# Kernel optimization log

Hardware: AMD Instinct MI355X
Metric: run time of the kernel (lower is better)

## Reference

```python
import jax, jax.numpy as jnp
import numpy as np

NEG = -1e30  # stands in for -inf on the diagonal; exp(NEG - max) == 0 exactly


def setup_inputs() -> dict:
    key = jax.random.key(0)
    k1, k2, k3, k4, k5 = jax.random.split(key, 5)
    B, C, H, W = 4, 512, 128, 128
    mid = C // 8  # 64
    x = jax.random.normal(k1, (B, C, H, W), dtype=jnp.float32)
    Wq = jax.random.normal(k2, (mid, C), dtype=jnp.float32) * (1.0 / np.sqrt(C))
    Wk = jax.random.normal(k3, (mid, C), dtype=jnp.float32) * (1.0 / np.sqrt(C))
    Wv = jax.random.normal(k4, (C, C), dtype=jnp.float32) * (1.0 / np.sqrt(C))
    gamma = jax.random.normal(k5, (1,), dtype=jnp.float32) * 0.1
    return {"x": x, "Wq": Wq, "Wk": Wk, "Wv": Wv, "gamma": gamma}


def reference(x, Wq, Wk, Wv, gamma):
    B, C, H, W = x.shape
    # 1x1 convs == channel matmuls
    q = jnp.einsum('bchw,mc->bmhw', x, Wq)  # (B, mid, H, W)
    k = jnp.einsum('bchw,mc->bmhw', x, Wk)
    v = jnp.einsum('bchw,dc->bdhw', x, Wv)  # (B, C, H, W)

    # vertical (H-axis) logits with -inf diagonal: eH[b,i,w,j] = sum_m q[b,m,i,w] k[b,m,j,w]
    eH = jnp.einsum('bmiw,bmjw->biwj', q, k)           # (B, H, W, H)
    diag = jnp.eye(H, dtype=bool)[:, None, :]          # (H, 1, H)
    eH = jnp.where(diag, NEG, eH)

    # horizontal (W-axis) logits: eW[b,h,i,j] = sum_m q[b,m,h,i] k[b,m,h,j]
    eW = jnp.einsum('bmhi,bmhj->bhij', q, k)           # (B, H, W, W)

    # joint softmax over the concatenated H+W logits
    attn = jax.nn.softmax(jnp.concatenate([eH, eW], axis=3), axis=3)  # (B, H, W, H+W)
    aH = attn[:, :, :, :H]  # (B, H, W, H)
    aW = attn[:, :, :, H:]  # (B, H, W, W)

    # attention-weighted value aggregation along each axis
    outH = jnp.einsum('bcjw,biwj->bciw', v, aH)  # (B, C, H, W)
    outW = jnp.einsum('bchj,bhij->bchi', v, aW)  # (B, C, H, W)

    return gamma[0] * (outH + outW) + x
```

## Files before the change

kernel.cpp:

```cpp
#include <hip/hip_runtime.h>
#include <cstdint>
#include <cstddef>

#define NEGV (-1e30f)

constexpr int C_ = 512, H_ = 128, W_ = 128;
constexpr int P_ = 16384;

typedef short bf16x8 __attribute__((ext_vector_type(8)));
typedef float f32x4  __attribute__((ext_vector_type(4)));
typedef _Float16 f16x4 __attribute__((ext_vector_type(4)));
#define MFMA16(a, b, c) __builtin_amdgcn_mfma_f32_16x16x32_bf16((a), (b), (c), 0, 0, 0)

#define SWZ128(r, cs) (((r) << 7) + (((((cs) >> 3) ^ ((r) & 7))) << 3) + ((cs) & 7))
#define SWZ64(r, cs)  (((r) << 6) + (((((cs) >> 3) ^ ((r) & 7))) << 3) + ((cs) & 7))

__device__ inline void gl_lds16(const void* g, void* l) {
    __builtin_amdgcn_global_load_lds(
        (const __attribute__((address_space(1))) unsigned int*)g,
        (__attribute__((address_space(3))) unsigned int*)l, 16, 0, 0);
}

__device__ inline unsigned short f2bf(float f) {
    union { float f; uint32_t i; } t; t.f = f;
    uint32_t r = t.i + 0x7FFFu + ((t.i >> 16) & 1u);
    return (unsigned short)(r >> 16);
}

__global__ __launch_bounds__(256) void kwconv(
    const float* __restrict__ Wq, const float* __restrict__ Wk,
    const float* __restrict__ Wv,
    unsigned short* __restrict__ Wqkbf, unsigned short* __restrict__ Wvbf)
{
    const int i4 = (blockIdx.x * 256 + threadIdx.x) * 4;
    const float* src; unsigned short* dst; int off;
    if (i4 < 32768)       { src = Wq + i4;          dst = Wqkbf + i4; }
    else if (i4 < 65536)  { off = i4 - 32768; src = Wk + off; dst = Wqkbf + i4; }
    else                  { off = i4 - 65536; src = Wv + off; dst = Wvbf + off; }
    const float4 v = *(const float4*)src;
    ushort4 u; u.x = f2bf(v.x); u.y = f2bf(v.y); u.z = f2bf(v.z); u.w = f2bf(v.w);
    *(ushort4*)dst = u;
}

__global__ __launch_bounds__(256) void kprep1(
    const float* __restrict__ x, unsigned short* __restrict__ xTbf)
{
    __shared__ float t[32][33];
    const int tid = threadIdx.x;
    const int h0 = (blockIdx.x >> 2) * 32, w0 = (blockIdx.x & 3) * 32;
    const size_t base = (size_t)blockIdx.y * P_;
    {
        const int r = tid >> 3, c4 = (tid & 7) * 4;
        const float4 v = *(const float4*)&x[base + (size_t)(h0 + r) * 128 + w0 + c4];
        t[r][c4] = v.x; t[r][c4 + 1] = v.y; t[r][c4 + 2] = v.z; t[r][c4 + 3] = v.w;
    }
    __syncthreads();
    {
        const int wr = tid >> 3, hc = (tid & 7) * 4;
        ushort4 u;
        u.x = f2bf(t[hc][wr]);     u.y = f2bf(t[hc + 1][wr]);
        u.z = f2bf(t[hc + 2][wr]); u.w = f2bf(t[hc + 3][wr]);
        *(ushort4*)&xTbf[base + (size_t)(w0 + wr) * 128 + h0 + hc] = u;
    }
}

__global__ __launch_bounds__(256) void kprep2(
    const float* __restrict__ x, unsigned short* __restrict__ xbfT)
{
    __shared__ float t[32][33];
    const int tid = threadIdx.x;
    const int p0 = blockIdx.x * 32, c0 = blockIdx.y * 32, b = blockIdx.z;
    {
        const int r = tid >> 3, c4 = (tid & 7) * 4;
        const float4 v = *(const float4*)&x[((size_t)(b * C_ + c0 + r)) * P_ + p0 + c4];
        t[r][c4] = v.x; t[r][c4 + 1] = v.y; t[r][c4 + 2] = v.z; t[r][c4 + 3] = v.w;
    }
    __syncthreads();
    {
        const int pr = tid >> 3, cc = (tid & 7) * 4;
        ushort4 u;
        u.x = f2bf(t[cc][pr]);     u.y = f2bf(t[cc + 1][pr]);
        u.z = f2bf(t[cc + 2][pr]); u.w = f2bf(t[cc + 3][pr]);
        *(ushort4*)&xbfT[((size_t)b * P_ + p0 + pr) * C_ + c0 + cc] = u;
    }
}

__global__ __launch_bounds__(256) void kgemmqk(
    const unsigned short* __restrict__ A, const unsigned short* __restrict__ Bm,
    unsigned short* __restrict__ outbf)
{
    __shared__ __attribute__((aligned(16))) unsigned short sA[2][128 * 64];
    __shared__ __attribute__((aligned(16))) unsigned short sB[2][128 * 64];
    const int tid = threadIdx.x;
    const int pbase = blockIdx.x * 128, b = blockIdx.z;
    const int lane = tid & 63, wv = tid >> 6;
    const int m0 = (wv >> 1) * 64, p0 = (wv & 1) * 64;
    const int fr = lane & 15, fq = lane >> 4;

    f32x4 acc[4][4];
#pragma unroll
    for (int i = 0; i < 4; i++)
#pragma unroll
        for (int j = 0; j < 4; j++) acc[i][j] = (f32x4){0.f, 0.f, 0.f, 0.f};

    const size_t brow0 = ((size_t)b * P_ + pbase) * 512;

#define QK_STAGE(chunk, buf) {                                                  \
        const int kc_ = (chunk) * 64;                                           \
        _Pragma("unroll")                                                       \
        for (int rep = 0; rep < 4; rep++) {                                     \
            const int idx = rep * 256 + tid;                                    \
            const int r_ = idx >> 3, kgs = (idx & 7) ^ (r_ & 7);                \
            gl_lds16(&A[(size_t)r_ * 512 + kc_ + kgs * 8], &sA[buf][idx * 8]);  \
            gl_lds16(&Bm[brow0 + (size_t)r_ * 512 + kc_ + kgs * 8], &sB[buf][idx * 8]); \
        } }

    QK_STAGE(0, 0);
    int cur = 0;
    for (int chunk = 0; chunk < 8; ++chunk) {
        if (chunk < 7) {
            QK_STAGE(chunk + 1, cur ^ 1);
            asm volatile("s_waitcnt vmcnt(8)" ::: "memory");
        } else {
            asm volatile("s_waitcnt vmcnt(0)" ::: "memory");
        }
        __builtin_amdgcn_s_barrier();
#pragma unroll
        for (int kk = 0; kk < 64; kk += 32) {
            bf16x8 af[4], bfv[4];
#pragma unroll
            for (int t = 0; t < 4; t++) af[t]  = *(const bf16x8*)&sA[cur][SWZ64(m0 + t * 16 + fr, kk + fq * 8)];
#pragma unroll
            for (int t = 0; t < 4; t++) bfv[t] = *(const bf16x8*)&sB[cur][SWZ64(p0 + t * 16 + fr, kk + fq * 8)];
#pragma unroll
            for (int i = 0; i < 4; i++)
#pragma unroll
                for (int j = 0; j < 4; j++)
                    acc[i][j] = MFMA16(af[i], bfv[j], acc[i][j]);
        }
        if (chunk < 7) __builtin_amdgcn_s_barrier();
        cur ^= 1;
    }
#undef QK_STAGE

#pragma unroll
    for (int tj = 0; tj < 4; tj++) {
        const int p_g = pbase + p0 + tj * 16 + fr;
        const size_t rowo = ((size_t)b * P_ + p_g) * 128;
#pragma unroll
        for (int ti = 0; ti < 4; ti++) {
            const int mk = m0 + ti * 16 + fq * 4;
            ushort4 u;
            u.x = f2bf(acc[ti][tj][0]); u.y = f2bf(acc[ti][tj][1]);
            u.z = f2bf(acc[ti][tj][2]); u.w = f2bf(acc[ti][tj][3]);
            *(ushort4*)&outbf[rowo + mk] = u;
        }
    }
}

__global__ __launch_bounds__(256) void klogits(
    const unsigned short* __restrict__ qkP,
    _Float16* __restrict__ ERow, _Float16* __restrict__ ECol)
{
    __shared__ __attribute__((aligned(16))) unsigned short sPM[128 * 136];
    const int tid = threadIdx.x;
    const int s = blockIdx.x, b = blockIdx.y, mode = blockIdx.z;
    const int rowMul  = mode ? 1 : 128;
    const int rowStep = mode ? 128 : 1;
    _Float16* E = mode ? ECol : ERow;
    const size_t qbase = (size_t)b * P_ * 128;
    const int rb = s * rowMul;
#pragma unroll
    for (int rep = 0; rep < 8; rep++) {
        const int idx = rep * 256 + tid;
        const int mkg = idx & 15, i = idx >> 4;
        *(uint4*)&sPM[i * 136 + mkg * 8] =
            *(const uint4*)&qkP[qbase + (size_t)(rb + i * rowStep) * 128 + mkg * 8];
    }
    __syncthreads();

    const int lane = tid & 63, wv = tid >> 6;
    const int i0 = (wv >> 1) * 64, j0 = (wv & 1) * 64;
    const int fr = lane & 15, fq = lane >> 4;

    f32x4 acc[4][4];
#pragma unroll
    for (int i = 0; i < 4; i++)
#pragma unroll
        for (int j = 0; j < 4; j++) acc[i][j] = (f32x4){0.f, 0.f, 0.f, 0.f};

#pragma unroll
    for (int kk = 0; kk < 64; kk += 32) {
        bf16x8 af[4], bfv[4];
#pragma unroll
        for (int t = 0; t < 4; t++) af[t]  = *(const bf16x8*)&sPM[(i0 + t * 16 + fr) * 136 + kk + fq * 8];
#pragma unroll
        for (int t = 0; t < 4; t++) bfv[t] = *(const bf16x8*)&sPM[(j0 + t * 16 + fr) * 136 + 64 + kk + fq * 8];
#pragma unroll
        for (int i = 0; i < 4; i++)
#pragma unroll
            for (int j = 0; j < 4; j++)
                acc[i][j] = MFMA16(af[i], bfv[j], acc[i][j]);
    }

    _Float16* Eb = E + ((size_t)(b * 128 + s)) * P_;
#pragma unroll
    for (int ti = 0; ti < 4; ti++)
#pragma unroll
        for (int r = 0; r < 4; r++) {
            const int i_g = i0 + ti * 16 + fq * 4 + r;
#pragma unroll
            for (int tj = 0; tj < 4; tj++) {
                const int j_g = j0 + tj * 16 + fr;
                float v = acc[ti][tj][r];
                if (mode && i_g == j_g) v = -60000.0f;
                Eb[(size_t)i_g * 128 + j_g] = (_Float16)v;
            }
        }
}

__global__ __launch_bounds__(256) void ksoftmax(
    const _Float16* __restrict__ ER, const _Float16* __restrict__ EC,
    unsigned short* __restrict__ AR, unsigned short* __restrict__ AC)
{
    const int tid = threadIdx.x;
    const int l32 = tid & 31;
    const int pix = blockIdx.x * 8 + (tid >> 5);
    const int b = pix >> 14, rem = pix & 16383;
    const int h = rem >> 7, w = rem & 127;
    const size_t ro = ((size_t)((b * 128 + h) * 128 + w)) * 128;
    const size_t co = ((size_t)((b * 128 + w) * 128 + h)) * 128;
    const f16x4 r = *(const f16x4*)(ER + ro + l32 * 4);
    const f16x4 c = *(const f16x4*)(EC + co + l32 * 4);
    const float r0 = r.x, r1 = r.y, r2 = r.z, r3 = r.w;
    const float c0 = c.x, c1 = c.y, c2 = c.z, c3 = c.w;
    float mx = fmaxf(fmaxf(fmaxf(r0, r1), fmaxf(r2, r3)),
                     fmaxf(fmaxf(c0, c1), fmaxf(c2, c3)));
#pragma unroll
    for (int off = 16; off > 0; off >>= 1) mx = fmaxf(mx, __shfl_xor(mx, off));
    const float e0 = __expf(r0 - mx), e1 = __expf(r1 - mx);
    const float e2 = __expf(r2 - mx), e3 = __expf(r3 - mx);
    const float f0 = __expf(c0 - mx), f1 = __expf(c1 - mx);
    const float f2 = __expf(c2 - mx), f3 = __expf(c3 - mx);
    float sm = (e0 + e1 + e2 + e3) + (f0 + f1 + f2 + f3);
#pragma unroll
    for (int off = 16; off > 0; off >>= 1) sm += __shfl_xor(sm, off);
    const float inv = 1.0f / sm;
    ushort4 u0, u1;
    u0.x = f2bf(e0 * inv); u0.y = f2bf(e1 * inv); u0.z = f2bf(e2 * inv); u0.w = f2bf(e3 * inv);
    u1.x = f2bf(f0 * inv); u1.y = f2bf(f1 * inv); u1.z = f2bf(f2 * inv); u1.w = f2bf(f3 * inv);
    *(ushort4*)(AR + ro + l32 * 4) = u0;
    *(ushort4*)(AC + co + l32 * 4) = u1;
}

__global__ __launch_bounds__(256) void kagg2(
    const unsigned short* __restrict__ ARow, const unsigned short* __restrict__ ACol,
    const float* __restrict__ x, const unsigned short* __restrict__ xTbf,
    unsigned short* __restrict__ ySumR, unsigned short* __restrict__ ySumC)
{
    __shared__ __attribute__((aligned(16))) unsigned short sAttn[128 * 128];
    __shared__ __attribute__((aligned(16))) unsigned short sX[128 * 128];
    const int tid = threadIdx.x;
    const int s = blockIdx.x, b = blockIdx.y, mode = blockIdx.z;
    const int lane = tid & 63, wv = tid >> 6;
    const int m0 = (wv >> 1) * 64, n0 = (wv & 1) * 64;
    const int fr = lane & 15, fq = lane >> 4;

    const unsigned short* At = (mode ? ACol : ARow) + ((size_t)(b * 128 + s)) * P_;
#pragma unroll
    for (int rep = 0; rep < 8; rep++) {
        const int idx = rep * 256 + tid;
        const int r = idx >> 4, sl = idx & 15;
        gl_lds16(&At[(size_t)r * 128 + (sl ^ (r & 7)) * 8], &sAttn[idx * 8]);
    }

    unsigned short* yS = mode ? ySumC : ySumR;

    for (int ct = 0; ct < 4; ct++) {
        if (mode == 0) {
            const float* Xf = &x[((size_t)(b * C_ + ct * 128)) * P_ + s * 128];
#pragma unroll
            for (int rep = 0; rep < 16; rep++) {
                const int idx = rep * 256 + tid;
                const int jq = idx & 31, cc = idx >> 5;
                const float4 v = *(const float4*)&Xf[(size_t)cc * P_ + jq * 4];
                ushort4 u; u.x = f2bf(v.x); u.y = f2bf(v.y); u.z = f2bf(v.z); u.w = f2bf(v.w);
                *(ushort4*)&sX[SWZ128(cc, jq * 4)] = u;
            }
        } else {
            const unsigned short* Xs = &xTbf[((size_t)(b * C_ + ct * 128)) * P_ + s * 128];
#pragma unroll
            for (int rep = 0; rep < 8; rep++) {
                const int idx = rep * 256 + tid;
                const int r = idx >> 4, sl = idx & 15;
                gl_lds16(&Xs[(size_t)r * P_ + (sl ^ (r & 7)) * 8], &sX[idx * 8]);
            }
        }
        __syncthreads();

        f32x4 acc[4][4];
#pragma unroll
        for (int i = 0; i < 4; i++)
#pragma unroll
            for (int j = 0; j < 4; j++) acc[i][j] = (f32x4){0.f, 0.f, 0.f, 0.f};

#pragma unroll
        for (int kk = 0; kk < 128; kk += 32) {
            bf16x8 af[4], bfv[4];
#pragma unroll
            for (int t = 0; t < 4; t++) {
                const int rc = m0 + t * 16 + fr;
                af[t] = *(const bf16x8*)&sX[SWZ128(rc, kk + fq * 8)];
            }
#pragma unroll
            for (int t = 0; t < 4; t++) {
                const int ri = n0 + t * 16 + fr;
                bfv[t] = *(const bf16x8*)&sAttn[SWZ128(ri, kk + fq * 8)];
            }
#pragma unroll
            for (int i = 0; i < 4; i++)
#pragma unroll
                for (int j = 0; j < 4; j++)
                    acc[i][j] = MFMA16(af[i], bfv[j], acc[i][j]);
        }

        const int cg0 = ct * 128 + m0 + fq * 4;
#pragma unroll
        for (int tj = 0; tj < 4; tj++) {
            const int i_g = n0 + tj * 16 + fr;
            const size_t p = mode ? ((size_t)i_g * 128 + s) : ((size_t)s * 128 + i_g);
            unsigned short* rowp = yS + ((size_t)b * P_ + p) * 512;
#pragma unroll
            for (int ti = 0; ti < 4; ti++) {
                ushort4 u;
                u.x = f2bf(acc[ti][tj][0]); u.y = f2bf(acc[ti][tj][1]);
                u.z = f2bf(acc[ti][tj][2]); u.w = f2bf(acc[ti][tj][3]);
                *(ushort4*)&rowp[cg0 + ti * 16] = u;
            }
        }
        __syncthreads();
    }
}

__global__ __launch_bounds__(512, 2) void kfinal256(
    const unsigned short* __restrict__ Wvbf,
    const unsigned short* __restrict__ yR,
    const unsigned short* __restrict__ yC,
    float* __restrict__ outf,
    const float* __restrict__ addx,
    const float* __restrict__ gammap)
{
    __shared__ __attribute__((aligned(16))) unsigned short sM[2][256 * 64];
    __shared__ __attribute__((aligned(16))) unsigned short sP[2][256 * 64];
    const int tid = threadIdx.x;
    const int pbase = blockIdx.x * 256, mt = blockIdx.y, b = blockIdx.z;
    const int lane = tid & 63, wv = tid >> 6;
    const int m0w = (wv >> 2) * 128;
    const int p0w = (wv & 3) * 64;
    const int fr = lane & 15, fq = lane >> 4;

    f32x4 acc[4][8];
#pragma unroll
    for (int i = 0; i < 4; i++)
#pragma unroll
        for (int j = 0; j < 8; j++) acc[i][j] = (f32x4){0.f, 0.f, 0.f, 0.f};

    const unsigned short* Arow = Wvbf + (size_t)(mt * 256) * 512;
    const size_t brow = ((size_t)b * P_ + pbase) * 512;

#define FIN_STAGE(chunk, buf) {                                                 \
        const int kc_ = ((chunk) & 7) * 64;                                     \
        const unsigned short* Bp = ((chunk) < 8 ? yR : yC) + brow + kc_;        \
        const unsigned short* Ap = Arow + kc_;                                  \
        _Pragma("unroll")                                                       \
        for (int rep = 0; rep < 4; rep++) {                                     \
            const int idx = rep * 512 + tid;                                    \
            const int r_ = idx >> 3, kgs = (idx & 7) ^ (r_ & 7);                \
            gl_lds16(&Ap[(size_t)r_ * 512 + kgs * 8], &sM[buf][idx * 8]);       \
            gl_lds16(&Bp[(size_t)r_ * 512 + kgs * 8], &sP[buf][idx * 8]);       \
        } }

    FIN_STAGE(0, 0);
    int cur = 0;
    for (int chunk = 0; chunk < 16; ++chunk) {
        if (chunk < 15) {
            FIN_STAGE(chunk + 1, cur ^ 1);
            asm volatile("s_waitcnt vmcnt(8)" ::: "memory");
        } else {
            asm volatile("s_waitcnt vmcnt(0)" ::: "memory");
        }
        __builtin_amdgcn_s_barrier();
#pragma unroll
        for (int kk = 0; kk < 64; kk += 32) {
            bf16x8 bp[4], am[8];
#pragma unroll
            for (int t = 0; t < 4; t++) bp[t] = *(const bf16x8*)&sP[cur][SWZ64(p0w + t * 16 + fr, kk + fq * 8)];
#pragma unroll
            for (int t = 0; t < 8; t++) am[t] = *(const bf16x8*)&sM[cur][SWZ64(m0w + t * 16 + fr, kk + fq * 8)];
            __builtin_amdgcn_s_setprio(1);
#pragma unroll
            for (int i = 0; i < 4; i++)
#pragma unroll
                for (int j = 0; j < 8; j++)
                    acc[i][j] = MFMA16(bp[i], am[j], acc[i][j]);
            __builtin_amdgcn_s_setprio(0);
        }
        if (chunk < 15) __builtin_amdgcn_s_barrier();
        cur ^= 1;
    }
#undef FIN_STAGE

    const float g = gammap[0];
#pragma unroll
    for (int ti = 0; ti < 4; ti++) {
        const int p_g = pbase + p0w + ti * 16 + fq * 4;
#pragma unroll
        for (int tj = 0; tj < 8; tj++) {
            const int m_g = mt * 256 + m0w + tj * 16 + fr;
            const size_t off = ((size_t)(b * 512 + m_g)) * P_ + p_g;
            const float4 xa = *(const float4*)&addx[off];
            float4 o;
            o.x = fmaf(g, acc[ti][tj][0], xa.x);
            o.y = fmaf(g, acc[ti][tj][1], xa.y);
            o.z = fmaf(g, acc[ti][tj][2], xa.z);
            o.w = fmaf(g, acc[ti][tj][3], xa.w);
            *(float4*)&outf[off] = o;
        }
    }
}

extern "C" void kernel_launch(void* const* d_in, const int* in_sizes, int n_in,
                              void* d_out, int out_size, void* d_ws, size_t ws_size,
                              hipStream_t stream) {
    const float* x     = (const float*)d_in[0];
    const float* Wq    = (const float*)d_in[1];
    const float* Wk    = (const float*)d_in[2];
    const float* Wv    = (const float*)d_in[3];
    const float* gamma = (const float*)d_in[4];
    float* out = (float*)d_out;

    char* base = (char*)d_ws;
    unsigned short* Wqkbf = (unsigned short*)base;             base += 131072;
    unsigned short* Wvbf  = (unsigned short*)base;             base += 524288;
    unsigned short* xTbf  = (unsigned short*)base;             base += 67108864;
    unsigned short* xbfT  = (unsigned short*)base;             base += 67108864;
    unsigned short* qkP   = (unsigned short*)base;             base += 16777216;
    _Float16*       ERow  = (_Float16*)base;                   base += 33554432;
    _Float16*       ECol  = (_Float16*)base;                   base += 33554432;
    unsigned short* ARow  = (unsigned short*)base;             base += 16777216;
    unsigned short* ACol  = (unsigned short*)base;             base += 16777216;
    unsigned short* ySumR = (unsigned short*)base;             base += 67108864;
    unsigned short* ySumC = (unsigned short*)ERow;

    kwconv<<<320, 256, 0, stream>>>(Wq, Wk, Wv, Wqkbf, Wvbf);
    kprep1<<<dim3(16, 2048), 256, 0, stream>>>(x, xTbf);
    kprep2<<<dim3(512, 16, 4), 256, 0, stream>>>(x, xbfT);
    kgemmqk<<<dim3(128, 1, 4), 256, 0, stream>>>(Wqkbf, xbfT, qkP);
    klogits<<<dim3(128, 4, 2), 256, 0, stream>>>(qkP, ERow, ECol);
    ksoftmax<<<8192, 256, 0, stream>>>(ERow, ECol, ARow, ACol);
    kagg2<<<dim3(128, 4, 2), 256, 0, stream>>>(ARow, ACol, x, xTbf, ySumR, ySumC);
    kfinal256<<<dim3(64, 2, 4), 512, 0, stream>>>(Wvbf, ySumR, ySumC, out, x, gamma);
}
```

Measured before the change: 517.7 us.

## Precompute bf16 x for row aggregation and restructure final GEMM to full-M tiles

kprep1 now also writes a bf16 copy of x in its natural layout when the workspace is large enough. kagg2 mode 0 can then load it with direct global-to-LDS copies instead of loading fp32 and converting. The final projection kernel is rewritten so each block covers all 512 output channels for 128 pixels. This removes the duplicated y reads across the two channel halves, but it drops the double-buffered prefetch pipeline in favour of synchronous load-then-compute with two barriers per chunk. It also adds 64MB of extra bf16 writes in prep and relies on the workspace having spare room.

```diff
diff --git a/kernel.cpp b/kernel.cpp
--- a/kernel.cpp
+++ b/kernel.cpp
@@ -43,7 +43,8 @@
 }
 
 __global__ __launch_bounds__(256) void kprep1(
-    const float* __restrict__ x, unsigned short* __restrict__ xTbf)
+    const float* __restrict__ x, unsigned short* __restrict__ xTbf,
+    unsigned short* __restrict__ xbf)
 {
     __shared__ float t[32][33];
     const int tid = threadIdx.x;
@@ -53,6 +54,10 @@
         const int r = tid >> 3, c4 = (tid & 7) * 4;
         const float4 v = *(const float4*)&x[base + (size_t)(h0 + r) * 128 + w0 + c4];
         t[r][c4] = v.x; t[r][c4 + 1] = v.y; t[r][c4 + 2] = v.z; t[r][c4 + 3] = v.w;
+        if (xbf) {
+            ushort4 u; u.x = f2bf(v.x); u.y = f2bf(v.y); u.z = f2bf(v.z); u.w = f2bf(v.w);
+            *(ushort4*)&xbf[base + (size_t)(h0 + r) * 128 + w0 + c4] = u;
+        }
     }
     __syncthreads();
     {
@@ -255,7 +260,8 @@
 
 __global__ __launch_bounds__(256) void kagg2(
     const unsigned short* __restrict__ ARow, const unsigned short* __restrict__ ACol,
-    const float* __restrict__ x, const unsigned short* __restrict__ xTbf,
+    const float* __restrict__ x, const unsigned short* __restrict__ xbf,
+    const unsigned short* __restrict__ xTbf,
     unsigned short* __restrict__ ySumR, unsigned short* __restrict__ ySumC)
 {
     __shared__ __attribute__((aligned(16))) unsigned short sAttn[128 * 128];
@@ -275,9 +281,18 @@
     }
 
     unsigned short* yS = mode ? ySumC : ySumR;
+    const unsigned short* Xsrc = mode ? xTbf : xbf;
 
     for (int ct = 0; ct < 4; ct++) {
-        if (mode == 0) {
+        if (Xsrc) {
+            const unsigned short* Xs = &Xsrc[((size_t)(b * C_ + ct * 128)) * P_ + s * 128];
+#pragma unroll
+            for (int rep = 0; rep < 8; rep++) {
+                const int idx = rep * 256 + tid;
+                const int r = idx >> 4, sl = idx & 15;
+                gl_lds16(&Xs[(size_t)r * P_ + (sl ^ (r & 7)) * 8], &sX[idx * 8]);
+            }
+        } else {
             const float* Xf = &x[((size_t)(b * C_ + ct * 128)) * P_ + s * 128];
 #pragma unroll
             for (int rep = 0; rep < 16; rep++) {
@@ -287,14 +302,6 @@
                 ushort4 u; u.x = f2bf(v.x); u.y = f2bf(v.y); u.z = f2bf(v.z); u.w = f2bf(v.w);
                 *(ushort4*)&sX[SWZ128(cc, jq * 4)] = u;
             }
-        } else {
-            const unsigned short* Xs = &xTbf[((size_t)(b * C_ + ct * 128)) * P_ + s * 128];
-#pragma unroll
-            for (int rep = 0; rep < 8; rep++) {
-                const int idx = rep * 256 + tid;
-                const int r = idx >> 4, sl = idx & 15;
-                gl_lds16(&Xs[(size_t)r * P_ + (sl ^ (r & 7)) * 8], &sX[idx * 8]);
-            }
         }
         __syncthreads();
 
@@ -342,7 +349,7 @@
     }
 }
 
-__global__ __launch_bounds__(512, 2) void kfinal256(
+__global__ __launch_bounds__(512) void kfinalM(
     const unsigned short* __restrict__ Wvbf,
     const unsigned short* __restrict__ yR,
     const unsigned short* __restrict__ yC,
@@ -350,13 +357,13 @@
     const float* __restrict__ addx,
     const float* __restrict__ gammap)
 {
-    __shared__ __attribute__((aligned(16))) unsigned short sM[2][256 * 64];
-    __shared__ __attribute__((aligned(16))) unsigned short sP[2][256 * 64];
-    const int tid = threadIdx.x;
-    const int pbase = blockIdx.x * 256, mt = blockIdx.y, b = blockIdx.z;
+    __shared__ __attribute__((aligned(16))) unsigned short sM[512 * 64];
+    __shared__ __attribute__((aligned(16))) unsigned short sP[128 * 64];
+    const int tid = threadIdx.x;
+    const int pbase = blockIdx.x * 128, b = blockIdx.z;
     const int lane = tid & 63, wv = tid >> 6;
-    const int m0w = (wv >> 2) * 128;
-    const int p0w = (wv & 3) * 64;
+    const int m0w = (wv >> 1) * 128;
+    const int p0w = (wv & 1) * 64;
     const int fr = lane & 15, fq = lane >> 4;
 
     f32x4 acc[4][8];
@@ -365,38 +372,33 @@
 #pragma unroll
         for (int j = 0; j < 8; j++) acc[i][j] = (f32x4){0.f, 0.f, 0.f, 0.f};
 
-    const unsigned short* Arow = Wvbf + (size_t)(mt * 256) * 512;
     const size_t brow = ((size_t)b * P_ + pbase) * 512;
 
-#define FIN_STAGE(chunk, buf) {                                                 \
-        const int kc_ = ((chunk) & 7) * 64;                                     \
-        const unsigned short* Bp = ((chunk) < 8 ? yR : yC) + brow + kc_;        \
-        const unsigned short* Ap = Arow + kc_;                                  \
-        _Pragma("unroll")                                                       \
-        for (int rep = 0; rep < 4; rep++) {                                     \
-            const int idx = rep * 512 + tid;                                    \
-            const int r_ = idx >> 3, kgs = (idx & 7) ^ (r_ & 7);                \
-            gl_lds16(&Ap[(size_t)r_ * 512 + kgs * 8], &sM[buf][idx * 8]);       \
-            gl_lds16(&Bp[(size_t)r_ * 512 + kgs * 8], &sP[buf][idx * 8]);       \
-        } }
-
-    FIN_STAGE(0, 0);
-    int cur = 0;
-    for (int chunk = 0; chunk < 16; ++chunk) {
-        if (chunk < 15) {
-            FIN_STAGE(chunk + 1, cur ^ 1);
-            asm volatile("s_waitcnt vmcnt(8)" ::: "memory");
-        } else {
-            asm volatile("s_waitcnt vmcnt(0)" ::: "memory");
-        }
-        __builtin_amdgcn_s_barrier();
+    for (int hc = 0; hc < 16; ++hc) {
+        const int kc = (hc >> 1) * 64;
+        const unsigned short* Bsrc = (hc & 1) ? yC : yR;
+        if (!(hc & 1)) {
+#pragma unroll
+            for (int rep = 0; rep < 8; rep++) {
+                const int idx = rep * 512 + tid;
+                const int r_ = idx >> 3, kgs = (idx & 7) ^ (r_ & 7);
+                gl_lds16(&Wvbf[(size_t)r_ * 512 + kc + kgs * 8], &sM[idx * 8]);
+            }
+        }
+#pragma unroll
+        for (int rep = 0; rep < 2; rep++) {
+            const int idx = rep * 512 + tid;
+            const int r_ = idx >> 3, kgs = (idx & 7) ^ (r_ & 7);
+            gl_lds16(&Bsrc[brow + (size_t)r_ * 512 + kc + kgs * 8], &sP[idx * 8]);
+        }
+        __syncthreads();
 #pragma unroll
         for (int kk = 0; kk < 64; kk += 32) {
             bf16x8 bp[4], am[8];
 #pragma unroll
-            for (int t = 0; t < 4; t++) bp[t] = *(const bf16x8*)&sP[cur][SWZ64(p0w + t * 16 + fr, kk + fq * 8)];
-#pragma unroll
-            for (int t = 0; t < 8; t++) am[t] = *(const bf16x8*)&sM[cur][SWZ64(m0w + t * 16 + fr, kk + fq * 8)];
+            for (int t = 0; t < 4; t++) bp[t] = *(const bf16x8*)&sP[SWZ64(p0w + t * 16 + fr, kk + fq * 8)];
+#pragma unroll
+            for (int t = 0; t < 8; t++) am[t] = *(const bf16x8*)&sM[SWZ64(m0w + t * 16 + fr, kk + fq * 8)];
             __builtin_amdgcn_s_setprio(1);
 #pragma unroll
             for (int i = 0; i < 4; i++)
@@ -405,10 +407,8 @@
                     acc[i][j] = MFMA16(bp[i], am[j], acc[i][j]);
             __builtin_amdgcn_s_setprio(0);
         }
-        if (chunk < 15) __builtin_amdgcn_s_barrier();
-        cur ^= 1;
-    }
-#undef FIN_STAGE
+        __syncthreads();
+    }
 
     const float g = gammap[0];
 #pragma unroll
@@ -416,7 +416,7 @@
         const int p_g = pbase + p0w + ti * 16 + fq * 4;
 #pragma unroll
         for (int tj = 0; tj < 8; tj++) {
-            const int m_g = mt * 256 + m0w + tj * 16 + fr;
+            const int m_g = m0w + tj * 16 + fr;
             const size_t off = ((size_t)(b * 512 + m_g)) * P_ + p_g;
             const float4 xa = *(const float4*)&addx[off];
             float4 o;
@@ -451,13 +451,16 @@
     unsigned short* ACol  = (unsigned short*)base;             base += 16777216;
     unsigned short* ySumR = (unsigned short*)base;             base += 67108864;
     unsigned short* ySumC = (unsigned short*)ERow;
+    const size_t used = (size_t)(base - (char*)d_ws);
+    unsigned short* xbf = nullptr;
+    if (ws_size >= used + 67108864) { xbf = (unsigned short*)base; base += 67108864; }
 
     kwconv<<<320, 256, 0, stream>>>(Wq, Wk, Wv, Wqkbf, Wvbf);
-    kprep1<<<dim3(16, 2048), 256, 0, stream>>>(x, xTbf);
+    kprep1<<<dim3(16, 2048), 256, 0, stream>>>(x, xTbf, xbf);
     kprep2<<<dim3(512, 16, 4), 256, 0, stream>>>(x, xbfT);
     kgemmqk<<<dim3(128, 1, 4), 256, 0, stream>>>(Wqkbf, xbfT, qkP);
     klogits<<<dim3(128, 4, 2), 256, 0, stream>>>(qkP, ERow, ECol);
     ksoftmax<<<8192, 256, 0, stream>>>(ERow, ECol, ARow, ACol);
-    kagg2<<<dim3(128, 4, 2), 256, 0, stream>>>(ARow, ACol, x, xTbf, ySumR, ySumC);
-    kfinal256<<<dim3(64, 2, 4), 512, 0, stream>>>(Wvbf, ySumR, ySumC, out, x, gamma);
-}
+    kagg2<<<dim3(128, 4, 2), 256, 0, stream>>>(ARow, ACol, x, xbf, xTbf, ySumR, ySumC);
+    kfinalM<<<dim3(128, 1, 4), 512, 0, stream>>>(Wvbf, ySumR, ySumC, out, x, gamma);
+}
```

New measurement: 543.1 us. 4.9% more time.
